# Performance work log

Measured on AMD Instinct MI355X. Metric: run time of the kernel, lower is better.

## Reference

```python
import jax, jax.numpy as jnp
import numpy as np

ALPHA = 0.2  # LeakyReLU negative slope
NEG_INF = -9e15


def setup_inputs() -> dict:
    key = jax.random.key(0)
    k1, k2, k3, k4 = jax.random.split(key, 4)
    M, N, Fin, Fout = 32, 1024, 128, 128
    h = jax.random.normal(k1, (M, N, Fin), dtype=jnp.float32)
    adj = jax.random.randint(k2, (M, N, N), 0, 2, dtype=jnp.int32)
    W = jax.random.normal(k3, (Fin, Fout), dtype=jnp.float32) * (1.414 * (6.0 / (Fin + Fout)) ** 0.5)
    a = jax.random.normal(k4, (2 * Fout, 1), dtype=jnp.float32) * (1.414 * (6.0 / (2 * Fout + 1)) ** 0.5)
    return {"h": h, "adj": adj, "W": W, "a": a}


def reference(h, adj, W, a):
    # Wh: [M, N, Fout]
    Wh = jnp.einsum('mnf,fo->mno', h, W)
    Fout = W.shape[1]
    # Algebraic decomposition of concat([Wh_i, Wh_j]) @ a:
    # a_input[m,i,j] @ a == Wh[m,i]@a[:Fout] + Wh[m,j]@a[Fout:]
    e_src = Wh @ a[:Fout, 0]   # [M, N]
    e_dst = Wh @ a[Fout:, 0]   # [M, N]
    e = e_src[:, :, None] + e_dst[:, None, :]      # [M, N, N]
    e = jnp.where(e > 0, e, ALPHA * e)             # LeakyReLU
    masked = jnp.where(adj > 0, e, NEG_INF)
    # NOTE: original softmaxes over dim=1 (faithful reproduction)
    attention = jax.nn.softmax(masked, axis=1)
    # dropout is a no-op in eval mode
    h_prime = jnp.einsum('mij,mjo->mio', attention, Wh)
    return jax.nn.elu(h_prime)  # concat=True branch
```

## Files before the change

### kernel.cpp

```cpp
#include <hip/hip_runtime.h>
#include <hip/hip_bf16.h>
#include <hip/hip_cooperative_groups.h>

namespace cg = cooperative_groups;

typedef __attribute__((ext_vector_type(4))) float f32x4;
typedef __attribute__((ext_vector_type(8))) short short8;
typedef __attribute__((ext_vector_type(4))) int i32x4;

#define ALPHA 0.2f
#define NEG_BIG -9e15f

static __device__ __forceinline__ short f2bf(float f) {
    __hip_bfloat16 b = __float2bfloat16(f);
    return __builtin_bit_cast(short, b);
}

#define MFMA16(A, B, C) __builtin_amdgcn_mfma_f32_16x16x32_bf16((A), (B), (C), 0, 0, 0)

struct SA { short Wt[128 * 136]; float la[256]; float lws[128]; float lwd[128]; };
struct SB { int buf[2][4096]; float les[128]; float red[8]; };
struct SC { short Bt[2][128 * 40]; float led[1024]; float lc[1024]; float ld[1024]; float red[8]; };

__global__ __launch_bounds__(256) void gat_mega(
        const float* __restrict__ h, const int* __restrict__ adj,
        const float* __restrict__ W, const float* __restrict__ a,
        short* __restrict__ whbt, float* __restrict__ es, float* __restrict__ ed,
        unsigned long long* __restrict__ bits, float* __restrict__ spart,
        float* __restrict__ out) {
    __shared__ __align__(16) char smem[36864];
    cg::grid_group grid = cg::this_grid();
    const int b = blockIdx.x;
    const int tid = threadIdx.x;
    const int w = tid >> 6, l = tid & 63;
    const int q = l >> 4, cl = l & 15;
    const int m = b >> 3, sub = b & 7;
    const int T0 = sub * 128;

    {
        SA* S = (SA*)smem;
        S->la[tid] = a[tid];
        __syncthreads();
        {
            const int k = tid >> 1, hh = tid & 1;
            const float* wr = W + k * 128 + hh * 64;
            float ps = 0.f, pd = 0.f;
            #pragma unroll
            for (int f = 0; f < 64; f += 4) {
                f32x4 wv = *(const f32x4*)(wr + f);
                #pragma unroll
                for (int e = 0; e < 4; ++e) {
                    ps += wv[e] * S->la[hh * 64 + f + e];
                    pd += wv[e] * S->la[128 + hh * 64 + f + e];
                }
            }
            ps += __shfl_xor(ps, 1);
            pd += __shfl_xor(pd, 1);
            if (hh == 0) { S->lws[k] = ps; S->lwd[k] = pd; }
        }
        #pragma unroll 4
        for (int i = 0; i < 64; ++i) {
            int idx = i * 256 + tid;
            int kk = idx >> 7, o = idx & 127;
            S->Wt[o * 136 + kk] = f2bf(W[idx]);
        }
        __syncthreads();
        const int row0 = T0 + w * 32 + cl;
        f32x4 acc[2][8];
        const f32x4 vz = {0.f, 0.f, 0.f, 0.f};
        #pragma unroll
        for (int i = 0; i < 2; ++i)
            #pragma unroll
            for (int j = 0; j < 8; ++j) acc[i][j] = vz;
        float esp0 = 0.f, edp0 = 0.f, esp1 = 0.f, edp1 = 0.f;
        const float* hrow0 = h + ((size_t)m * 1024 + row0) * 128;
        const float* hrow1 = hrow0 + 16 * 128;
        #pragma unroll
        for (int kk = 0; kk < 128; kk += 32) {
            const int kb = kk + q * 8;
            f32x4 wsA = *(const f32x4*)&S->lws[kb], wsB = *(const f32x4*)&S->lws[kb + 4];
            f32x4 wdA = *(const f32x4*)&S->lwd[kb], wdB = *(const f32x4*)&S->lwd[kb + 4];
            f32x4 h0a = *(const f32x4*)(hrow0 + kb), h0b = *(const f32x4*)(hrow0 + kb + 4);
            f32x4 h1a = *(const f32x4*)(hrow1 + kb), h1b = *(const f32x4*)(hrow1 + kb + 4);
            short8 af0, af1;
            #pragma unroll
            for (int e = 0; e < 4; ++e) {
                esp0 += h0a[e] * wsA[e] + h0b[e] * wsB[e];
                edp0 += h0a[e] * wdA[e] + h0b[e] * wdB[e];
                esp1 += h1a[e] * wsA[e] + h1b[e] * wsB[e];
                edp1 += h1a[e] * wdA[e] + h1b[e] * wdB[e];
                af0[e] = f2bf(h0a[e]); af0[e + 4] = f2bf(h0b[e]);
                af1[e] = f2bf(h1a[e]); af1[e + 4] = f2bf(h1b[e]);
            }
            #pragma unroll
            for (int nf = 0; nf < 8; ++nf) {
                short8 bf = *(const short8*)&S->Wt[(nf * 16 + cl) * 136 + kb];
                acc[0][nf] = MFMA16(af0, bf, acc[0][nf]);
                acc[1][nf] = MFMA16(af1, bf, acc[1][nf]);
            }
        }
        {
            float v0 = esp0; v0 += __shfl_xor(v0, 16); v0 += __shfl_xor(v0, 32);
            float u0 = edp0; u0 += __shfl_xor(u0, 16); u0 += __shfl_xor(u0, 32);
            float v1 = esp1; v1 += __shfl_xor(v1, 16); v1 += __shfl_xor(v1, 32);
            float u1 = edp1; u1 += __shfl_xor(u1, 16); u1 += __shfl_xor(u1, 32);
            if (q == 0) {
                es[m * 1024 + row0] = v0;       ed[m * 1024 + row0] = u0;
                es[m * 1024 + row0 + 16] = v1;  ed[m * 1024 + row0 + 16] = u1;
            }
        }
        #pragma unroll
        for (int mf = 0; mf < 2; ++mf) {
            const int rowb = T0 + w * 32 + mf * 16 + q * 4;
            #pragma unroll
            for (int nf = 0; nf < 8; ++nf) {
                const int o = nf * 16 + cl;
                size_t base = ((size_t)m * 128 + o) * 1024 + rowb;
                #pragma unroll
                for (int r = 0; r < 4; r += 2) {
                    unsigned lo = (unsigned short)f2bf(acc[mf][nf][r]);
                    unsigned hi = (unsigned short)f2bf(acc[mf][nf][r + 1]);
                    *(unsigned*)(whbt + base + r) = lo | (hi << 16);
                }
            }
        }
    }
    __threadfence();
    grid.sync();

    {
        SB* S = (SB*)smem;
        {
            f32x4 ev = *(const f32x4*)&es[m * 1024 + tid * 4];
            float mx = fmaxf(fmaxf(ev[0], ev[1]), fmaxf(ev[2], ev[3]));
            #pragma unroll
            for (int d = 1; d < 64; d <<= 1) mx = fmaxf(mx, __shfl_xor(mx, d));
            if (l == 0) S->red[w] = mx;
        }
        const size_t gr2 = (size_t)m * 1024 + T0;
        if (tid < 128) S->les[tid] = es[gr2 + tid];
        __syncthreads();
        const float Ma = fmaxf(fmaxf(S->red[0], S->red[1]), fmaxf(S->red[2], S->red[3]));
        const int j0 = tid * 4;
        const f32x4 edv = *(const f32x4*)&ed[m * 1024 + j0];
        float ub[4], sr[4] = {0.f, 0.f, 0.f, 0.f};
        #pragma unroll
        for (int e = 0; e < 4; ++e) {
            float x = Ma + edv[e];
            ub[e] = fmaxf(x, ALPHA * x);
        }
        auto issue = [&](int s) {
            const int row = s * 4 + w;
            const int* gp = adj + (gr2 + row) * 1024 + l * 4;
            int* dst = &S->buf[s & 1][w * 1024];
            #pragma unroll
            for (int k = 0; k < 4; ++k)
                __builtin_amdgcn_global_load_lds(
                    (const __attribute__((address_space(1))) void*)(gp + k * 256),
                    (__attribute__((address_space(3))) void*)(dst + k * 256), 16, 0, 0);
        };
        issue(0);
        #pragma unroll 1
        for (int s = 0; s < 32; ++s) {
            if (s < 31) {
                issue(s + 1);
                asm volatile("s_waitcnt vmcnt(16)" ::: "memory");
            } else {
                asm volatile("s_waitcnt vmcnt(0)" ::: "memory");
            }
            __builtin_amdgcn_s_barrier();
            const int* bufc = S->buf[s & 1];
            unsigned long long* bprow = bits + (gr2 + (size_t)s * 4) * 16 + w * 4;
            #pragma unroll
            for (int r = 0; r < 4; ++r) {
                const i32x4 av = *(const i32x4*)&bufc[r * 1024 + j0];
                unsigned long long b0 = __ballot(av[0] != 0);
                unsigned long long b1 = __ballot(av[1] != 0);
                unsigned long long b2 = __ballot(av[2] != 0);
                unsigned long long b3 = __ballot(av[3] != 0);
                if (l == 0) {
                    ulonglong2 p0; p0.x = b0; p0.y = b1;
                    ulonglong2 p1; p1.x = b2; p1.y = b3;
                    *(ulonglong2*)(bprow + (size_t)r * 16) = p0;
                    *(ulonglong2*)(bprow + (size_t)r * 16 + 2) = p1;
                }
                const float esb = S->les[s * 4 + r];
                #pragma unroll
                for (int e = 0; e < 4; ++e) {
                    float x = esb + edv[e];
                    float lk = fmaxf(x, ALPHA * x);
                    float t = __expf(lk - ub[e]);
                    sr[e] += (av[e] != 0) ? t : 0.f;
                }
            }
            __builtin_amdgcn_s_barrier();
        }
        f32x4 s4; s4[0] = sr[0]; s4[1] = sr[1]; s4[2] = sr[2]; s4[3] = sr[3];
        *(f32x4*)&spart[((size_t)(m * 8 + sub)) * 1024 + j0] = s4;
    }
    __threadfence();
    grid.sync();

    {
        SC* S = (SC*)smem;
        {
            f32x4 ev = *(const f32x4*)&es[m * 1024 + tid * 4];
            float mx = fmaxf(fmaxf(ev[0], ev[1]), fmaxf(ev[2], ev[3]));
            #pragma unroll
            for (int d = 1; d < 64; d <<= 1) mx = fmaxf(mx, __shfl_xor(mx, d));
            if (l == 0) S->red[w] = mx;
        }
        __syncthreads();
        const float Ma = fmaxf(fmaxf(S->red[0], S->red[1]), fmaxf(S->red[2], S->red[3]));
        const int j0 = tid * 4;
        {
            f32x4 Sv = {0.f, 0.f, 0.f, 0.f};
            const float* sp = spart + (size_t)m * 8 * 1024 + j0;
            #pragma unroll
            for (int it = 0; it < 8; ++it) Sv += *(const f32x4*)(sp + it * 1024);
            f32x4 edv4 = *(const f32x4*)&ed[m * 1024 + j0];
            #pragma unroll
            for (int e = 0; e < 4; ++e) {
                float x = Ma + edv4[e];
                float ubv = fmaxf(x, ALPHA * x);
                bool dead = !(Sv[e] > 0.f);
                S->led[j0 + e] = edv4[e];
                S->lc[j0 + e] = dead ? NEG_BIG : ubv;
                S->ld[j0 + e] = dead ? (1.0f / 1024.0f) : 1.0f / Sv[e];
            }
        }
        const int row0 = T0 + w * 32 + cl;
        const float es0 = es[m * 1024 + row0];
        const float es1 = es[m * 1024 + row0 + 16];
        const unsigned long long* bp0 = bits + ((size_t)m * 1024 + row0) * 16;
        const unsigned long long* bp1 = bp0 + 16 * 16;
        f32x4 acc[2][8];
        const f32x4 vz = {0.f, 0.f, 0.f, 0.f};
        #pragma unroll
        for (int i = 0; i < 2; ++i)
            #pragma unroll
            for (int jx = 0; jx < 8; ++jx) acc[i][jx] = vz;
        const int so = tid >> 1, sh = tid & 1;
        const short* gsrc = whbt + ((size_t)m * 128 + so) * 1024 + sh * 16;
        short* dst0 = &S->Bt[0][so * 40 + sh * 16];
        {
            uint4 r0 = *(const uint4*)gsrc;
            uint4 r1 = *(const uint4*)(gsrc + 8);
            *(uint4*)dst0 = r0;
            *(uint4*)(dst0 + 8) = r1;
        }
        __syncthreads();
        int cur = 0;
        ulonglong2 wa0, wb0, wa1, wb1;
        wa0.x = wa0.y = wb0.x = wb0.y = 0ull;
        wa1.x = wa1.y = wb1.x = wb1.y = 0ull;
        #pragma unroll 2
        for (int kt = 0; kt < 32; ++kt) {
            const int jb = kt * 32 + q * 8;
            if ((kt & 7) == 0) {
                const ulonglong2* q0p = (const ulonglong2*)(bp0 + (kt >> 3) * 4);
                wa0 = q0p[0]; wb0 = q0p[1];
                const ulonglong2* q1p = (const ulonglong2*)(bp1 + (kt >> 3) * 4);
                wa1 = q1p[0]; wb1 = q1p[1];
            }
            uint4 n0, n1;
            if (kt < 31) {
                const short* g2 = gsrc + (kt + 1) * 32;
                n0 = *(const uint4*)g2;
                n1 = *(const uint4*)(g2 + 8);
            }
            const f32x4 edA = *(const f32x4*)&S->led[jb], edB = *(const f32x4*)&S->led[jb + 4];
            const f32x4 cA = *(const f32x4*)&S->lc[jb],   cB = *(const f32x4*)&S->lc[jb + 4];
            const f32x4 dA = *(const f32x4*)&S->ld[jb],   dB = *(const f32x4*)&S->ld[jb + 4];
            const int bbase = ((kt & 7) << 3) + (q << 1);
            short8 af0, af1;
            #pragma unroll
            for (int e = 0; e < 8; ++e) {
                const float edvv = (e < 4) ? edA[e] : edB[e - 4];
                const float cv = (e < 4) ? cA[e] : cB[e - 4];
                const float dv = (e < 4) ? dA[e] : dB[e - 4];
                const float x0 = es0 + edvv, x1 = es1 + edvv;
                const float l0 = fmaxf(x0, ALPHA * x0), l1 = fmaxf(x1, ALPHA * x1);
                const int bi = bbase + (e >> 2);
                const unsigned long long q0w = (e & 3) == 0 ? wa0.x : (e & 3) == 1 ? wa0.y
                                             : (e & 3) == 2 ? wb0.x : wb0.y;
                const unsigned long long q1w = (e & 3) == 0 ? wa1.x : (e & 3) == 1 ? wa1.y
                                             : (e & 3) == 2 ? wb1.x : wb1.y;
                const float m0 = ((q0w >> bi) & 1ull) ? l0 : NEG_BIG;
                const float m1 = ((q1w >> bi) & 1ull) ? l1 : NEG_BIG;
                af0[e] = f2bf(__expf(m0 - cv) * dv);
                af1[e] = f2bf(__expf(m1 - cv) * dv);
            }
            #pragma unroll
            for (int nf = 0; nf < 8; ++nf) {
                short8 bf = *(const short8*)&S->Bt[cur][(nf * 16 + cl) * 40 + q * 8];
                acc[0][nf] = MFMA16(af0, bf, acc[0][nf]);
                acc[1][nf] = MFMA16(af1, bf, acc[1][nf]);
            }
            if (kt < 31) {
                short* d2 = &S->Bt[cur ^ 1][so * 40 + sh * 16];
                *(uint4*)d2 = n0;
                *(uint4*)(d2 + 8) = n1;
                cur ^= 1;
            }
            __syncthreads();
        }
        #pragma unroll
        for (int mf = 0; mf < 2; ++mf) {
            const int rowb = T0 + w * 32 + mf * 16 + q * 4;
            #pragma unroll
            for (int nf = 0; nf < 8; ++nf) {
                const int o = nf * 16 + cl;
                #pragma unroll
                for (int r = 0; r < 4; ++r) {
                    const float v = acc[mf][nf][r];
                    const float evv = v > 0.f ? v : (__expf(v) - 1.0f);
                    out[((size_t)m * 1024 + rowb + r) * 128 + o] = evv;
                }
            }
        }
    }
}

__global__ __launch_bounds__(128) void k00_wsd(const float* __restrict__ W,
                                               const float* __restrict__ a,
                                               float* __restrict__ wsv,
                                               float* __restrict__ wdv) {
    int k = blockIdx.x, t = threadIdx.x;
    float v = W[k * 128 + t];
    float ps = v * a[t];
    float pd = v * a[128 + t];
    #pragma unroll
    for (int d = 1; d < 64; d <<= 1) {
        ps += __shfl_xor(ps, d);
        pd += __shfl_xor(pd, d);
    }
    __shared__ float tmp[4];
    if ((t & 63) == 0) { tmp[(t >> 6) * 2] = ps; tmp[(t >> 6) * 2 + 1] = pd; }
    __syncthreads();
    if (t == 0) { wsv[k] = tmp[0] + tmp[2]; wdv[k] = tmp[1] + tmp[3]; }
}

__global__ __launch_bounds__(256) void k0_wh(const float* __restrict__ h,
                                             const float* __restrict__ W,
                                             const float* __restrict__ wsv,
                                             const float* __restrict__ wdv,
                                             short* __restrict__ whbt,
                                             float* __restrict__ es,
                                             float* __restrict__ ed) {
    __shared__ __align__(16) short Wt[128 * 136];
    __shared__ __align__(16) float lws[128], lwd[128];
    const int tid = threadIdx.x;
    const int m = blockIdx.x >> 3, rt = blockIdx.x & 7;
    const int R0 = rt * 128;
    #pragma unroll 4
    for (int i = 0; i < 64; ++i) {
        int idx = i * 256 + tid;
        int k = idx >> 7, o = idx & 127;
        Wt[o * 136 + k] = f2bf(W[idx]);
    }
    if (tid < 128) { lws[tid] = wsv[tid]; lwd[tid] = wdv[tid]; }
    __syncthreads();
    const int w = tid >> 6, l = tid & 63;
    const int q = l >> 4, c = l & 15;
    const int row0 = R0 + w * 32 + c;
    f32x4 acc[2][8];
    const f32x4 vzero = {0.f, 0.f, 0.f, 0.f};
    #pragma unroll
    for (int i = 0; i < 2; ++i)
        #pragma unroll
        for (int j = 0; j < 8; ++j) acc[i][j] = vzero;
    float esp0 = 0.f, edp0 = 0.f, esp1 = 0.f, edp1 = 0.f;
    const float* hrow0 = h + ((size_t)m * 1024 + row0) * 128;
    const float* hrow1 = hrow0 + 16 * 128;
    #pragma unroll
    for (int kk = 0; kk < 128; kk += 32) {
        const int kb = kk + q * 8;
        f32x4 wsA = *(const f32x4*)&lws[kb], wsB = *(const f32x4*)&lws[kb + 4];
        f32x4 wdA = *(const f32x4*)&lwd[kb], wdB = *(const f32x4*)&lwd[kb + 4];
        f32x4 h0a = *(const f32x4*)(hrow0 + kb), h0b = *(const f32x4*)(hrow0 + kb + 4);
        f32x4 h1a = *(const f32x4*)(hrow1 + kb), h1b = *(const f32x4*)(hrow1 + kb + 4);
        short8 af0, af1;
        #pragma unroll
        for (int e = 0; e < 4; ++e) {
            esp0 += h0a[e] * wsA[e] + h0b[e] * wsB[e];
            edp0 += h0a[e] * wdA[e] + h0b[e] * wdB[e];
            esp1 += h1a[e] * wsA[e] + h1b[e] * wsB[e];
            edp1 += h1a[e] * wdA[e] + h1b[e] * wdB[e];
            af0[e] = f2bf(h0a[e]); af0[e + 4] = f2bf(h0b[e]);
            af1[e] = f2bf(h1a[e]); af1[e + 4] = f2bf(h1b[e]);
        }
        #pragma unroll
        for (int nf = 0; nf < 8; ++nf) {
            short8 bf = *(const short8*)&Wt[(nf * 16 + c) * 136 + kb];
            acc[0][nf] = MFMA16(af0, bf, acc[0][nf]);
            acc[1][nf] = MFMA16(af1, bf, acc[1][nf]);
        }
    }
    {
        float v0 = esp0; v0 += __shfl_xor(v0, 16); v0 += __shfl_xor(v0, 32);
        float u0 = edp0; u0 += __shfl_xor(u0, 16); u0 += __shfl_xor(u0, 32);
        float v1 = esp1; v1 += __shfl_xor(v1, 16); v1 += __shfl_xor(v1, 32);
        float u1 = edp1; u1 += __shfl_xor(u1, 16); u1 += __shfl_xor(u1, 32);
        if (q == 0) {
            es[m * 1024 + row0] = v0;       ed[m * 1024 + row0] = u0;
            es[m * 1024 + row0 + 16] = v1;  ed[m * 1024 + row0 + 16] = u1;
        }
    }
    #pragma unroll
    for (int mf = 0; mf < 2; ++mf) {
        const int rowb = R0 + w * 32 + mf * 16 + q * 4;
        #pragma unroll
        for (int nf = 0; nf < 8; ++nf) {
            const int o = nf * 16 + c;
            size_t base = ((size_t)m * 128 + o) * 1024 + rowb;
            #pragma unroll
            for (int r = 0; r < 4; r += 2) {
                unsigned lo = (unsigned short)f2bf(acc[mf][nf][r]);
                unsigned hi = (unsigned short)f2bf(acc[mf][nf][r + 1]);
                *(unsigned*)(whbt + base + r) = lo | (hi << 16);
            }
        }
    }
}

__global__ __launch_bounds__(256) void k0m_max(const float* __restrict__ es,
                                               float* __restrict__ mall) {
    const int m = blockIdx.x, tid = threadIdx.x;
    float4 v = *(const float4*)&es[m * 1024 + tid * 4];
    float mx = fmaxf(fmaxf(v.x, v.y), fmaxf(v.z, v.w));
    #pragma unroll
    for (int d = 1; d < 64; d <<= 1) mx = fmaxf(mx, __shfl_xor(mx, d));
    __shared__ float t[4];
    if ((tid & 63) == 0) t[tid >> 6] = mx;
    __syncthreads();
    if (tid == 0) mall[m] = fmaxf(fmaxf(t[0], t[1]), fmaxf(t[2], t[3]));
}

__global__ __launch_bounds__(256) void k1_stats(const int* __restrict__ adj,
                                                const float* __restrict__ es,
                                                const float* __restrict__ ed,
                                                const float* __restrict__ mall,
                                                unsigned long long* __restrict__ bits,
                                                float* __restrict__ spart) {
    const int b = blockIdx.x;
    const int m = b >> 6, it = b & 63;
    const int tid = threadIdx.x;
    const int w = tid >> 6, l = tid & 63;
    const int j0 = tid * 4;
    const float Ma = mall[m];
    const float4 edv = *(const float4*)&ed[m * 1024 + j0];
    float ub[4];
    #pragma unroll
    for (int e = 0; e < 4; ++e) {
        float x = Ma + ((const float*)&edv)[e];
        ub[e] = fmaxf(x, ALPHA * x);
    }
    const int4* ap = (const int4*)(adj + ((size_t)m * 1024 + it * 16) * 1024) + tid;
    int4 av[16];
    #pragma unroll
    for (int r = 0; r < 16; ++r) av[r] = ap[(size_t)r * 256];
    unsigned long long* bp = bits + ((size_t)m * 1024 + it * 16) * 16 + w * 4;
    #pragma unroll
    for (int r = 0; r < 16; ++r) {
        unsigned long long b0 = __ballot(av[r].x != 0);
        unsigned long long b1 = __ballot(av[r].y != 0);
        unsigned long long b2 = __ballot(av[r].z != 0);
        unsigned long long b3 = __ballot(av[r].w != 0);
        if (l == 0) {
            ulonglong2 p0, p1;
            p0.x = b0; p0.y = b1; p1.x = b2; p1.y = b3;
            *(ulonglong2*)(bp + (size_t)r * 16) = p0;
            *(ulonglong2*)(bp + (size_t)r * 16 + 2) = p1;
        }
    }
    float sr[4] = {0.f, 0.f, 0.f, 0.f};
    const float* ep = es + m * 1024 + it * 16;
    #pragma unroll
    for (int r = 0; r < 16; ++r) {
        const float esb = ep[r];
        #pragma unroll
        for (int e = 0; e < 4; ++e) {
            float x = esb + ((const float*)&edv)[e];
            float lk = fmaxf(x, ALPHA * x);
            float t = __expf(lk - ub[e]);
            sr[e] += ((&av[r].x)[e] != 0) ? t : 0.f;
        }
    }
    float4 s4; s4.x = sr[0]; s4.y = sr[1]; s4.z = sr[2]; s4.w = sr[3];
    *(float4*)&spart[((size_t)(m * 64 + it)) * 1024 + j0] = s4;
}

__global__ __launch_bounds__(256) void k1b_combine(const float* __restrict__ spart,
                                                   const float* __restrict__ ed,
                                                   const float* __restrict__ mall,
                                                   float* __restrict__ cc,
                                                   float* __restrict__ dinv) {
    const int g = blockIdx.x * 256 + threadIdx.x;
    const int m = g >> 10, j = g & 1023;
    const float* sp = spart + (size_t)m * 64 * 1024 + j;
    float S = 0.f;
    #pragma unroll
    for (int it = 0; it < 64; ++it) S += sp[it * 1024];
    float x = mall[m] + ed[g];
    float ub = fmaxf(x, ALPHA * x);
    bool dead = !(S > 0.f);
    cc[g] = dead ? NEG_BIG : ub;
    dinv[g] = dead ? (1.0f / 1024.0f) : 1.0f / S;
}

__global__ __launch_bounds__(256) void k2_pv(const unsigned long long* __restrict__ bits,
                                             const short* __restrict__ whbt,
                                             const float* __restrict__ es,
                                             const float* __restrict__ ed,
                                             const float* __restrict__ cc,
                                             const float* __restrict__ dinv,
                                             float* __restrict__ out) {
    __shared__ __align__(16) short Bt[2][128 * 40];
    __shared__ __align__(16) float led[1024], lc[1024], ld[1024];
    const int tid = threadIdx.x;
    const int m = blockIdx.x >> 3, rt = blockIdx.x & 7;
    const int R0 = rt * 128;
    for (int i = tid; i < 1024; i += 256) {
        led[i] = ed[m * 1024 + i];
        lc[i] = cc[m * 1024 + i];
        ld[i] = dinv[m * 1024 + i];
    }
    const int w = tid >> 6, l = tid & 63, q = l >> 4, cl = l & 15;
    const int row0 = R0 + w * 32 + cl;
    const float es0 = es[m * 1024 + row0];
    const float es1 = es[m * 1024 + row0 + 16];
    const unsigned long long* bp0 = bits + ((size_t)m * 1024 + row0) * 16;
    const unsigned long long* bp1 = bp0 + 16 * 16;
    f32x4 acc[2][8];
    const f32x4 vzero = {0.f, 0.f, 0.f, 0.f};
    #pragma unroll
    for (int i = 0; i < 2; ++i)
        #pragma unroll
        for (int jx = 0; jx < 8; ++jx) acc[i][jx] = vzero;
    const int so = tid >> 1, sh = tid & 1;
    const short* gsrc = whbt + ((size_t)m * 128 + so) * 1024 + sh * 16;
    short* dst0 = &Bt[0][so * 40 + sh * 16];
    {
        uint4 r0 = *(const uint4*)gsrc;
        uint4 r1 = *(const uint4*)(gsrc + 8);
        *(uint4*)dst0 = r0;
        *(uint4*)(dst0 + 8) = r1;
    }
    __syncthreads();
    int cur = 0;
    ulonglong2 wa0, wb0, wa1, wb1;
    wa0.x = wa0.y = wb0.x = wb0.y = 0ull;
    wa1.x = wa1.y = wb1.x = wb1.y = 0ull;
    #pragma unroll 2
    for (int kt = 0; kt < 32; ++kt) {
        const int jb = kt * 32 + q * 8;
        if ((kt & 7) == 0) {
            const ulonglong2* q0 = (const ulonglong2*)(bp0 + (kt >> 3) * 4);
            wa0 = q0[0]; wb0 = q0[1];
            const ulonglong2* q1 = (const ulonglong2*)(bp1 + (kt >> 3) * 4);
            wa1 = q1[0]; wb1 = q1[1];
        }
        uint4 n0, n1;
        if (kt < 31) {
            const short* g2 = gsrc + (kt + 1) * 32;
            n0 = *(const uint4*)g2;
            n1 = *(const uint4*)(g2 + 8);
        }
        const f32x4 edA = *(const f32x4*)&led[jb], edB = *(const f32x4*)&led[jb + 4];
        const f32x4 cA = *(const f32x4*)&lc[jb],   cB = *(const f32x4*)&lc[jb + 4];
        const f32x4 dA = *(const f32x4*)&ld[jb],   dB = *(const f32x4*)&ld[jb + 4];
        const int bbase = ((kt & 7) << 3) + (q << 1);
        short8 af0, af1;
        #pragma unroll
        for (int e = 0; e < 8; ++e) {
            const float edv = (e < 4) ? edA[e] : edB[e - 4];
            const float cv = (e < 4) ? cA[e] : cB[e - 4];
            const float dv = (e < 4) ? dA[e] : dB[e - 4];
            const float x0 = es0 + edv, x1 = es1 + edv;
            const float l0 = fmaxf(x0, ALPHA * x0), l1 = fmaxf(x1, ALPHA * x1);
            const int bi = bbase + (e >> 2);
            const unsigned long long q0w = (e & 3) == 0 ? wa0.x : (e & 3) == 1 ? wa0.y
                                         : (e & 3) == 2 ? wb0.x : wb0.y;
            const unsigned long long q1w = (e & 3) == 0 ? wa1.x : (e & 3) == 1 ? wa1.y
                                         : (e & 3) == 2 ? wb1.x : wb1.y;
            const float m0 = ((q0w >> bi) & 1ull) ? l0 : NEG_BIG;
            const float m1 = ((q1w >> bi) & 1ull) ? l1 : NEG_BIG;
            af0[e] = f2bf(__expf(m0 - cv) * dv);
            af1[e] = f2bf(__expf(m1 - cv) * dv);
        }
        const short* bb = &Bt[cur][0];
        #pragma unroll
        for (int nf = 0; nf < 8; ++nf) {
            short8 bf = *(const short8*)&bb[(nf * 16 + cl) * 40 + q * 8];
            acc[0][nf] = MFMA16(af0, bf, acc[0][nf]);
            acc[1][nf] = MFMA16(af1, bf, acc[1][nf]);
        }
        if (kt < 31) {
            short* d2 = &Bt[cur ^ 1][so * 40 + sh * 16];
            *(uint4*)d2 = n0;
            *(uint4*)(d2 + 8) = n1;
            cur ^= 1;
        }
        __syncthreads();
    }
    #pragma unroll
    for (int mf = 0; mf < 2; ++mf) {
        const int rowb = R0 + w * 32 + mf * 16 + q * 4;
        #pragma unroll
        for (int nf = 0; nf < 8; ++nf) {
            const int o = nf * 16 + cl;
            #pragma unroll
            for (int r = 0; r < 4; ++r) {
                const float v = acc[mf][nf][r];
                const float evv = v > 0.f ? v : (__expf(v) - 1.0f);
                out[((size_t)m * 1024 + rowb + r) * 128 + o] = evv;
            }
        }
    }
}

extern "C" void kernel_launch(void* const* d_in, const int* in_sizes, int n_in,
                              void* d_out, int out_size, void* d_ws, size_t ws_size,
                              hipStream_t stream) {
    const float* h = (const float*)d_in[0];
    const int* adj = (const int*)d_in[1];
    const float* W = (const float*)d_in[2];
    const float* a = (const float*)d_in[3];
    float* out = (float*)d_out;

    char* p = (char*)d_ws;
    auto alloc = [&](size_t bytes) -> char* {
        char* r = p;
        p += (bytes + 255) & ~(size_t)255;
        return r;
    };
    short* whbt = (short*)alloc((size_t)32 * 128 * 1024 * 2);
    float* es = (float*)alloc((size_t)32 * 1024 * 4);
    float* ed = (float*)alloc((size_t)32 * 1024 * 4);
    float* wsv = (float*)alloc(128 * 4);
    float* wdv = (float*)alloc(128 * 4);
    float* mall = (float*)alloc(32 * 4);
    unsigned long long* bits = (unsigned long long*)alloc((size_t)32 * 1024 * 16 * 8);
    float* spart = (float*)alloc((size_t)32 * 64 * 1024 * 4);
    float* cc = (float*)alloc((size_t)32 * 1024 * 4);
    float* dinv = (float*)alloc((size_t)32 * 1024 * 4);

    int maxBlk = 0;
    hipError_t oe = hipOccupancyMaxActiveBlocksPerMultiprocessor(
        &maxBlk, (const void*)gat_mega, 256, 0);
    int numCU = 0;
    hipError_t ae = hipDeviceGetAttribute(&numCU, hipDeviceAttributeMultiprocessorCount, 0);
    bool useCoop = (oe == hipSuccess) && (ae == hipSuccess) &&
                   ((long long)maxBlk * numCU >= 256);

    if (useCoop) {
        void* kargs[] = { (void*)&h, (void*)&adj, (void*)&W, (void*)&a,
                          (void*)&whbt, (void*)&es, (void*)&ed, (void*)&bits,
                          (void*)&spart, (void*)&out };
        hipLaunchCooperativeKernel(reinterpret_cast<void*>(gat_mega), dim3(256), dim3(256),
                                   kargs, 0, stream);
    } else {
        k00_wsd<<<128, 128, 0, stream>>>(W, a, wsv, wdv);
        k0_wh<<<256, 256, 0, stream>>>(h, W, wsv, wdv, whbt, es, ed);
        k0m_max<<<32, 256, 0, stream>>>(es, mall);
        k1_stats<<<2048, 256, 0, stream>>>(adj, es, ed, mall, bits, spart);
        k1b_combine<<<128, 256, 0, stream>>>(spart, ed, mall, cc, dinv);
        k2_pv<<<256, 256, 0, stream>>>(bits, whbt, es, ed, cc, dinv, out);
    }
}
```

Measured before the change: 88.87 us.

## Split cooperative mega-kernel into 512 blocks of 64 rows each

The fused cooperative GAT kernel now launches 512 blocks that each own 64 rows of a batch, where it used to launch 256 blocks of 128 rows. Each wave handles one 16-row MFMA tile instead of two, and the stats phase loops 16 steps instead of 32, with the vmcnt wait and partial-sum layout adjusted to match. The goal is to fill more of the MI355X's CUs, since 256 blocks leave many idle. In exchange, each loaded WhT tile is reused by fewer rows, there are twice as many partial sums to combine, and the coop path needs 512 co-resident blocks. The W transpose stride in LDS also changes from 136 to 138 to alter bank mapping.

```diff
diff --git a/kernel.cpp b/kernel.cpp
--- a/kernel.cpp
+++ b/kernel.cpp
@@ -10,6 +10,7 @@
 
 #define ALPHA 0.2f
 #define NEG_BIG -9e15f
+#define WTP 138
 
 static __device__ __forceinline__ short f2bf(float f) {
     __hip_bfloat16 b = __float2bfloat16(f);
@@ -18,8 +19,8 @@
 
 #define MFMA16(A, B, C) __builtin_amdgcn_mfma_f32_16x16x32_bf16((A), (B), (C), 0, 0, 0)
 
-struct SA { short Wt[128 * 136]; float la[256]; float lws[128]; float lwd[128]; };
-struct SB { int buf[2][4096]; float les[128]; float red[8]; };
+struct SA { short Wt[128 * WTP]; float la[256]; float lws[128]; float lwd[128]; };
+struct SB { int buf[2][4096]; float les[64]; float red[8]; };
 struct SC { short Bt[2][128 * 40]; float led[1024]; float lc[1024]; float ld[1024]; float red[8]; };
 
 __global__ __launch_bounds__(256) void gat_mega(
@@ -28,14 +29,14 @@
         short* __restrict__ whbt, float* __restrict__ es, float* __restrict__ ed,
         unsigned long long* __restrict__ bits, float* __restrict__ spart,
         float* __restrict__ out) {
-    __shared__ __align__(16) char smem[36864];
+    __shared__ __align__(16) char smem[37632];
     cg::grid_group grid = cg::this_grid();
     const int b = blockIdx.x;
     const int tid = threadIdx.x;
     const int w = tid >> 6, l = tid & 63;
     const int q = l >> 4, cl = l & 15;
-    const int m = b >> 3, sub = b & 7;
-    const int T0 = sub * 128;
+    const int m = b >> 4, sub = b & 15;
+    const int T0 = sub * 64;
 
     {
         SA* S = (SA*)smem;
@@ -62,64 +63,53 @@
         for (int i = 0; i < 64; ++i) {
             int idx = i * 256 + tid;
             int kk = idx >> 7, o = idx & 127;
-            S->Wt[o * 136 + kk] = f2bf(W[idx]);
+            S->Wt[o * WTP + kk] = f2bf(W[idx]);
         }
         __syncthreads();
-        const int row0 = T0 + w * 32 + cl;
-        f32x4 acc[2][8];
+        const int row0 = T0 + w * 16 + cl;
+        f32x4 acc[8];
         const f32x4 vz = {0.f, 0.f, 0.f, 0.f};
         #pragma unroll
-        for (int i = 0; i < 2; ++i)
-            #pragma unroll
-            for (int j = 0; j < 8; ++j) acc[i][j] = vz;
-        float esp0 = 0.f, edp0 = 0.f, esp1 = 0.f, edp1 = 0.f;
+        for (int j = 0; j < 8; ++j) acc[j] = vz;
+        float esp0 = 0.f, edp0 = 0.f;
         const float* hrow0 = h + ((size_t)m * 1024 + row0) * 128;
-        const float* hrow1 = hrow0 + 16 * 128;
         #pragma unroll
         for (int kk = 0; kk < 128; kk += 32) {
             const int kb = kk + q * 8;
             f32x4 wsA = *(const f32x4*)&S->lws[kb], wsB = *(const f32x4*)&S->lws[kb + 4];
             f32x4 wdA = *(const f32x4*)&S->lwd[kb], wdB = *(const f32x4*)&S->lwd[kb + 4];
             f32x4 h0a = *(const f32x4*)(hrow0 + kb), h0b = *(const f32x4*)(hrow0 + kb + 4);
-            f32x4 h1a = *(const f32x4*)(hrow1 + kb), h1b = *(const f32x4*)(hrow1 + kb + 4);
-            short8 af0, af1;
+            short8 af0;
             #pragma unroll
             for (int e = 0; e < 4; ++e) {
                 esp0 += h0a[e] * wsA[e] + h0b[e] * wsB[e];
                 edp0 += h0a[e] * wdA[e] + h0b[e] * wdB[e];
-                esp1 += h1a[e] * wsA[e] + h1b[e] * wsB[e];
-                edp1 += h1a[e] * wdA[e] + h1b[e] * wdB[e];
                 af0[e] = f2bf(h0a[e]); af0[e + 4] = f2bf(h0b[e]);
-                af1[e] = f2bf(h1a[e]); af1[e + 4] = f2bf(h1b[e]);
             }
             #pragma unroll
             for (int nf = 0; nf < 8; ++nf) {
-                short8 bf = *(const short8*)&S->Wt[(nf * 16 + cl) * 136 + kb];
-                acc[0][nf] = MFMA16(af0, bf, acc[0][nf]);
-                acc[1][nf] = MFMA16(af1, bf, acc[1][nf]);
+                short8 bf = *(const short8*)&S->Wt[(nf * 16 + cl) * WTP + kb];
+                acc[nf] = MFMA16(af0, bf, acc[nf]);
             }
         }
         {
             float v0 = esp0; v0 += __shfl_xor(v0, 16); v0 += __shfl_xor(v0, 32);
             float u0 = edp0; u0 += __shfl_xor(u0, 16); u0 += __shfl_xor(u0, 32);
-            float v1 = esp1; v1 += __shfl_xor(v1, 16); v1 += __shfl_xor(v1, 32);
-            float u1 = edp1; u1 += __shfl_xor(u1, 16); u1 += __shfl_xor(u1, 32);
             if (q == 0) {
-                es[m * 1024 + row0] = v0;       ed[m * 1024 + row0] = u0;
-                es[m * 1024 + row0 + 16] = v1;  ed[m * 1024 + row0 + 16] = u1;
-            }
-        }
-        #pragma unroll
-        for (int mf = 0; mf < 2; ++mf) {
-            const int rowb = T0 + w * 32 + mf * 16 + q * 4;
+                es[m * 1024 + row0] = v0;
+                ed[m * 1024 + row0] = u0;
+            }
+        }
+        {
+            const int rowb = T0 + w * 16 + q * 4;
             #pragma unroll
             for (int nf = 0; nf < 8; ++nf) {
                 const int o = nf * 16 + cl;
                 size_t base = ((size_t)m * 128 + o) * 1024 + rowb;
                 #pragma unroll
                 for (int r = 0; r < 4; r += 2) {
-                    unsigned lo = (unsigned short)f2bf(acc[mf][nf][r]);
-                    unsigned hi = (unsigned short)f2bf(acc[mf][nf][r + 1]);
+                    unsigned lo = (unsigned short)f2bf(acc[nf][r]);
+                    unsigned hi = (unsigned short)f2bf(acc[nf][r + 1]);
                     *(unsigned*)(whbt + base + r) = lo | (hi << 16);
                 }
             }
@@ -138,7 +128,7 @@
             if (l == 0) S->red[w] = mx;
         }
         const size_t gr2 = (size_t)m * 1024 + T0;
-        if (tid < 128) S->les[tid] = es[gr2 + tid];
+        if (tid < 64) S->les[tid] = es[gr2 + tid];
         __syncthreads();
         const float Ma = fmaxf(fmaxf(S->red[0], S->red[1]), fmaxf(S->red[2], S->red[3]));
         const int j0 = tid * 4;
@@ -161,10 +151,10 @@
         };
         issue(0);
         #pragma unroll 1
-        for (int s = 0; s < 32; ++s) {
-            if (s < 31) {
+        for (int s = 0; s < 16; ++s) {
+            if (s < 15) {
                 issue(s + 1);
-                asm volatile("s_waitcnt vmcnt(16)" ::: "memory");
+                asm volatile("s_waitcnt vmcnt(4)" ::: "memory");
             } else {
                 asm volatile("s_waitcnt vmcnt(0)" ::: "memory");
             }
@@ -196,7 +186,7 @@
             __builtin_amdgcn_s_barrier();
         }
         f32x4 s4; s4[0] = sr[0]; s4[1] = sr[1]; s4[2] = sr[2]; s4[3] = sr[3];
-        *(f32x4*)&spart[((size_t)(m * 8 + sub)) * 1024 + j0] = s4;
+        *(f32x4*)&spart[((size_t)(m * 16 + sub)) * 1024 + j0] = s4;
     }
     __threadfence();
     grid.sync();
@@ -215,9 +205,9 @@
         const int j0 = tid * 4;
         {
             f32x4 Sv = {0.f, 0.f, 0.f, 0.f};
-            const float* sp = spart + (size_t)m * 8 * 1024 + j0;
-            #pragma unroll
-            for (int it = 0; it < 8; ++it) Sv += *(const f32x4*)(sp + it * 1024);
+            const float* sp = spart + (size_t)m * 16 * 1024 + j0;
+            #pragma unroll
+            for (int it = 0; it < 16; ++it) Sv += *(const f32x4*)(sp + it * 1024);
             f32x4 edv4 = *(const f32x4*)&ed[m * 1024 + j0];
             #pragma unroll
             for (int e = 0; e < 4; ++e) {
@@ -229,17 +219,13 @@
                 S->ld[j0 + e] = dead ? (1.0f / 1024.0f) : 1.0f / Sv[e];
             }
         }
-        const int row0 = T0 + w * 32 + cl;
+        const int row0 = T0 + w * 16 + cl;
         const float es0 = es[m * 1024 + row0];
-        const float es1 = es[m * 1024 + row0 + 16];
         const unsigned long long* bp0 = bits + ((size_t)m * 1024 + row0) * 16;
-        const unsigned long long* bp1 = bp0 + 16 * 16;
-        f32x4 acc[2][8];
+        f32x4 acc[8];
         const f32x4 vz = {0.f, 0.f, 0.f, 0.f};
         #pragma unroll
-        for (int i = 0; i < 2; ++i)
-            #pragma unroll
-            for (int jx = 0; jx < 8; ++jx) acc[i][jx] = vz;
+        for (int jx = 0; jx < 8; ++jx) acc[jx] = vz;
         const int so = tid >> 1, sh = tid & 1;
         const short* gsrc = whbt + ((size_t)m * 128 + so) * 1024 + sh * 16;
         short* dst0 = &S->Bt[0][so * 40 + sh * 16];
@@ -251,17 +237,14 @@
         }
         __syncthreads();
         int cur = 0;
-        ulonglong2 wa0, wb0, wa1, wb1;
+        ulonglong2 wa0, wb0;
         wa0.x = wa0.y = wb0.x = wb0.y = 0ull;
-        wa1.x = wa1.y = wb1.x = wb1.y = 0ull;
         #pragma unroll 2
         for (int kt = 0; kt < 32; ++kt) {
             const int jb = kt * 32 + q * 8;
             if ((kt & 7) == 0) {
                 const ulonglong2* q0p = (const ulonglong2*)(bp0 + (kt >> 3) * 4);
                 wa0 = q0p[0]; wb0 = q0p[1];
-                const ulonglong2* q1p = (const ulonglong2*)(bp1 + (kt >> 3) * 4);
-                wa1 = q1p[0]; wb1 = q1p[1];
             }
             uint4 n0, n1;
             if (kt < 31) {
@@ -273,29 +256,24 @@
             const f32x4 cA = *(const f32x4*)&S->lc[jb],   cB = *(const f32x4*)&S->lc[jb + 4];
             const f32x4 dA = *(const f32x4*)&S->ld[jb],   dB = *(const f32x4*)&S->ld[jb + 4];
             const int bbase = ((kt & 7) << 3) + (q << 1);
-            short8 af0, af1;
+            short8 af0;
             #pragma unroll
             for (int e = 0; e < 8; ++e) {
                 const float edvv = (e < 4) ? edA[e] : edB[e - 4];
                 const float cv = (e < 4) ? cA[e] : cB[e - 4];
                 const float dv = (e < 4) ? dA[e] : dB[e - 4];
-                const float x0 = es0 + edvv, x1 = es1 + edvv;
-                const float l0 = fmaxf(x0, ALPHA * x0), l1 = fmaxf(x1, ALPHA * x1);
+                const float x0 = es0 + edvv;
+                const float l0 = fmaxf(x0, ALPHA * x0);
                 const int bi = bbase + (e >> 2);
                 const unsigned long long q0w = (e & 3) == 0 ? wa0.x : (e & 3) == 1 ? wa0.y
                                              : (e & 3) == 2 ? wb0.x : wb0.y;
-                const unsigned long long q1w = (e & 3) == 0 ? wa1.x : (e & 3) == 1 ? wa1.y
-                                             : (e & 3) == 2 ? wb1.x : wb1.y;
                 const float m0 = ((q0w >> bi) & 1ull) ? l0 : NEG_BIG;
-                const float m1 = ((q1w >> bi) & 1ull) ? l1 : NEG_BIG;
                 af0[e] = f2bf(__expf(m0 - cv) * dv);
-                af1[e] = f2bf(__expf(m1 - cv) * dv);
             }
             #pragma unroll
             for (int nf = 0; nf < 8; ++nf) {
                 short8 bf = *(const short8*)&S->Bt[cur][(nf * 16 + cl) * 40 + q * 8];
-                acc[0][nf] = MFMA16(af0, bf, acc[0][nf]);
-                acc[1][nf] = MFMA16(af1, bf, acc[1][nf]);
+                acc[nf] = MFMA16(af0, bf, acc[nf]);
             }
             if (kt < 31) {
                 short* d2 = &S->Bt[cur ^ 1][so * 40 + sh * 16];
@@ -305,15 +283,14 @@
             }
             __syncthreads();
         }
-        #pragma unroll
-        for (int mf = 0; mf < 2; ++mf) {
-            const int rowb = T0 + w * 32 + mf * 16 + q * 4;
+        {
+            const int rowb = T0 + w * 16 + q * 4;
             #pragma unroll
             for (int nf = 0; nf < 8; ++nf) {
                 const int o = nf * 16 + cl;
                 #pragma unroll
                 for (int r = 0; r < 4; ++r) {
-                    const float v = acc[mf][nf][r];
+                    const float v = acc[nf][r];
                     const float evv = v > 0.f ? v : (__expf(v) - 1.0f);
                     out[((size_t)m * 1024 + rowb + r) * 128 + o] = evv;
                 }
@@ -652,13 +629,13 @@
     int numCU = 0;
     hipError_t ae = hipDeviceGetAttribute(&numCU, hipDeviceAttributeMultiprocessorCount, 0);
     bool useCoop = (oe == hipSuccess) && (ae == hipSuccess) &&
-                   ((long long)maxBlk * numCU >= 256);
+                   ((long long)maxBlk * numCU >= 512);
 
     if (useCoop) {
         void* kargs[] = { (void*)&h, (void*)&adj, (void*)&W, (void*)&a,
                           (void*)&whbt, (void*)&es, (void*)&ed, (void*)&bits,
                           (void*)&spart, (void*)&out };
-        hipLaunchCooperativeKernel(reinterpret_cast<void*>(gat_mega), dim3(256), dim3(256),
+        hipLaunchCooperativeKernel(reinterpret_cast<void*>(gat_mega), dim3(512), dim3(256),
                                    kargs, 0, stream);
     } else {
         k00_wsd<<<128, 128, 0, stream>>>(W, a, wsv, wdv);
```

Result: no change. 88.87 us (median of 2 runs) (+0.0%).
